# Performance work log

Hardware: AMD Instinct MI355X
Metric: run time of the kernel (lower is better)

## Reference

```python
import jax, jax.numpy as jnp
import numpy as np

S = 8192          # total tokens (8 images x 1024 patches)
DIM = 1280        # hidden_size
H = 16            # num_heads
DH = DIM // H     # head_dim = 80
N_SEG = 8         # number of image segments (equal-length)


def setup_inputs() -> dict:
    key = jax.random.key(0)
    ks = jax.random.split(key, 8)
    hidden_states = jax.random.normal(ks[0], (S, DIM), dtype=jnp.float32)
    ang = jax.random.uniform(ks[1], (S, DH), dtype=jnp.float32) * (2.0 * np.pi)
    cos = jnp.cos(ang)
    sin = jnp.sin(ang)
    cu_seqlens = (jnp.arange(N_SEG + 1, dtype=jnp.int32) * (S // N_SEG))
    qkv_w = jax.random.normal(ks[2], (3 * DIM, DIM), dtype=jnp.float32) * 0.02
    qkv_b = jax.random.normal(ks[3], (3 * DIM,), dtype=jnp.float32) * 0.02
    proj_w = jax.random.normal(ks[4], (DIM, DIM), dtype=jnp.float32) * 0.02
    proj_b = jax.random.normal(ks[5], (DIM,), dtype=jnp.float32) * 0.02
    return {
        "hidden_states": hidden_states,
        "cos": cos,
        "sin": sin,
        "qkv_w": qkv_w,
        "qkv_b": qkv_b,
        "proj_w": proj_w,
        "proj_b": proj_b,
        "cu_seqlens": cu_seqlens,
    }


def _rotate_half(x):
    d = x.shape[-1] // 2
    return jnp.concatenate([-x[..., d:], x[..., :d]], axis=-1)


def reference(hidden_states, cos, sin, qkv_w, qkv_b, proj_w, proj_b, cu_seqlens):
    s, dim = hidden_states.shape
    dh = cos.shape[-1]
    h = dim // dh
    n_seg = cu_seqlens.shape[0] - 1  # static; segments are equal-length
    L = s // n_seg
    scale = dh ** -0.5

    # fused QKV projection: [S, 3, H, DH]
    qkv = (hidden_states @ qkv_w.T + qkv_b).reshape(s, 3, h, dh)
    q, k, v = qkv[:, 0], qkv[:, 1], qkv[:, 2]

    # RoPE (fp32, broadcast cos/sin over heads)
    cos_b = cos[:, None, :].astype(jnp.float32)
    sin_b = sin[:, None, :].astype(jnp.float32)
    qf, kf = q.astype(jnp.float32), k.astype(jnp.float32)
    q = (qf * cos_b + _rotate_half(qf) * sin_b).astype(q.dtype)
    k = (kf * cos_b + _rotate_half(kf) * sin_b).astype(k.dtype)

    # per-segment (block-diagonal) attention: reshape to [n_seg, L, H, DH]
    qs = q.reshape(n_seg, L, h, dh)
    ks = k.reshape(n_seg, L, h, dh)
    vs = v.reshape(n_seg, L, h, dh)
    scores = jnp.einsum("glhd,gmhd->ghlm", qs, ks) * scale
    attn = jax.nn.softmax(scores, axis=-1)
    out = jnp.einsum("ghlm,gmhd->glhd", attn, vs).reshape(s, dim)
    return out @ proj_w.T + proj_b
```

## Files before the change

kernel.cpp:

```cpp
#include <hip/hip_runtime.h>
#include <hip/hip_bf16.h>
#include <stdint.h>

typedef unsigned short u16;
typedef unsigned int u32;
typedef __attribute__((ext_vector_type(8))) short short8;
typedef __attribute__((ext_vector_type(4))) float f32x4;

#define DEV __device__ __forceinline__

constexpr int S = 8192;
constexpr int DIM = 1280;
constexpr int H = 16;
constexpr int DH = 80;
constexpr int LSEG = 1024;
constexpr int QKVN = 3 * DIM;
constexpr float SCALE = 0.11180339887498949f * 1.4426950408889634f;

DEV u16 f2bf(float f) {
  u32 u = __float_as_uint(f);
  return (u16)((u + 0x7FFFu + ((u >> 16) & 1u)) >> 16);
}
DEV float bf2f(u16 h) { return __uint_as_float(((u32)h) << 16); }
DEV u32 pkbf(float a, float b) {
  __hip_bfloat162 t = __float22bfloat162_rn(float2{a, b});
  u32 r; __builtin_memcpy(&r, &t, 4); return r;
}

DEV void glds16(const void* g, void* l) {
  __builtin_amdgcn_global_load_lds((__attribute__((address_space(1))) void*)g,
                                   (__attribute__((address_space(3))) void*)l,
                                   16, 0, 0);
}
DEV f32x4 mfma16(short8 a, short8 b, f32x4 c) {
  return __builtin_amdgcn_mfma_f32_16x16x32_bf16(a, b, c, 0, 0, 0);
}

__global__ __launch_bounds__(256) void cvt_kernel(
    const float* __restrict__ X, const float* __restrict__ Wq,
    const float* __restrict__ Wp, u16* __restrict__ Xb,
    u16* __restrict__ Wqb, u16* __restrict__ Wpb) {
  size_t i = ((size_t)blockIdx.x * 256 + threadIdx.x) * 4;
  const size_t n1 = (size_t)S * DIM;
  const size_t n2 = (size_t)QKVN * DIM;
  const size_t n3 = (size_t)DIM * DIM;
  const float* src; u16* dst; size_t off;
  if (i < n1)                { src = X;  dst = Xb;  off = i; }
  else if (i < n1 + n2)      { src = Wq; dst = Wqb; off = i - n1; }
  else if (i < n1 + n2 + n3) { src = Wp; dst = Wpb; off = i - n1 - n2; }
  else return;
  float4 v = *(const float4*)(src + off);
  ushort4 r;
  r.x = f2bf(v.x); r.y = f2bf(v.y); r.z = f2bf(v.z); r.w = f2bf(v.w);
  *(ushort4*)(dst + off) = r;
}

__global__ __launch_bounds__(256) void rope_kernel(
    const u16* __restrict__ QKV, const float* __restrict__ cosp,
    const float* __restrict__ sinp, u16* __restrict__ Qp, u16* __restrict__ Kp) {
  int idx = blockIdx.x * 256 + threadIdx.x;
  int c = idx % 5;
  int sh = idx / 5;
  int s = sh >> 4, h = sh & 15;
  const size_t gbase = (size_t)s * QKVN + h * DH + c * 8;
  const size_t pbase = (size_t)sh * 96 + c * 8;
  short8 q0 = *(const short8*)&QKV[gbase];
  short8 q1 = *(const short8*)&QKV[gbase + 40];
  short8 k0 = *(const short8*)&QKV[gbase + DIM];
  short8 k1 = *(const short8*)&QKV[gbase + DIM + 40];
  float4 ca0 = *(const float4*)&cosp[s * DH + c * 8];
  float4 ca1 = *(const float4*)&cosp[s * DH + c * 8 + 4];
  float4 cb0 = *(const float4*)&cosp[s * DH + c * 8 + 40];
  float4 cb1 = *(const float4*)&cosp[s * DH + c * 8 + 44];
  float4 sa0 = *(const float4*)&sinp[s * DH + c * 8];
  float4 sa1 = *(const float4*)&sinp[s * DH + c * 8 + 4];
  float4 sb0 = *(const float4*)&sinp[s * DH + c * 8 + 40];
  float4 sb1 = *(const float4*)&sinp[s * DH + c * 8 + 44];
  float ca[8] = {ca0.x, ca0.y, ca0.z, ca0.w, ca1.x, ca1.y, ca1.z, ca1.w};
  float cb[8] = {cb0.x, cb0.y, cb0.z, cb0.w, cb1.x, cb1.y, cb1.z, cb1.w};
  float sa[8] = {sa0.x, sa0.y, sa0.z, sa0.w, sa1.x, sa1.y, sa1.z, sa1.w};
  float sb[8] = {sb0.x, sb0.y, sb0.z, sb0.w, sb1.x, sb1.y, sb1.z, sb1.w};
  short8 qo0, qo1, ko0, ko1;
#pragma unroll
  for (int j = 0; j < 8; j++) {
    float qa = bf2f((u16)q0[j]), qb = bf2f((u16)q1[j]);
    float ka = bf2f((u16)k0[j]), kb = bf2f((u16)k1[j]);
    qo0[j] = (short)f2bf((qa * ca[j] - qb * sa[j]) * SCALE);
    qo1[j] = (short)f2bf((qb * cb[j] + qa * sb[j]) * SCALE);
    ko0[j] = (short)f2bf(ka * ca[j] - kb * sa[j]);
    ko1[j] = (short)f2bf(kb * cb[j] + ka * sb[j]);
  }
  *(short8*)&Qp[pbase]      = qo0;
  *(short8*)&Qp[pbase + 40] = qo1;
  *(short8*)&Kp[pbase]      = ko0;
  *(short8*)&Kp[pbase + 40] = ko1;
  if (c == 0) {
    short8 z = {};
    *(short8*)&Qp[pbase + 80] = z; *(short8*)&Qp[pbase + 88] = z;
    *(short8*)&Kp[pbase + 80] = z; *(short8*)&Kp[pbase + 88] = z;
  }
}

__global__ __launch_bounds__(256) void vtrans_kernel(
    const u16* __restrict__ QKV, u16* __restrict__ Vt) {
  __shared__ u16 Ls[64 * 88];
  const int s0 = blockIdx.x * 64, h = blockIdx.y;
  const int tid = threadIdx.x;
  for (int cc = tid; cc < 640; cc += 256) {
    int row = cc / 10, c = cc % 10;
    short8 v = *(const short8*)&QKV[(size_t)(s0 + row) * QKVN + 2 * DIM + h * 80 + c * 8];
    *(short8*)&Ls[row * 88 + c * 8] = v;
  }
  __syncthreads();
  for (int cc = tid; cc < 640; cc += 256) {
    int d = cc / 8, sc = cc % 8;
    u16 tmp[8];
#pragma unroll
    for (int j = 0; j < 8; j++) {
      int op = sc * 8 + j;
      int key = ((op & 3) << 4) + (op >> 2);
      tmp[j] = Ls[key * 88 + d];
    }
    *(short8*)&Vt[(size_t)(h * 80 + d) * S + s0 + sc * 8] = *(short8*)tmp;
  }
}

template <bool OUT_F32>
__global__ __launch_bounds__(512, 2) void gemm_bt(
    const u16* __restrict__ A, const u16* __restrict__ B,
    const float* __restrict__ bias, void* __restrict__ C, int K, int N) {
  __shared__ u16 As[2][2][8192];
  __shared__ u16 Bs[2][2][8192];
  const int ntn = N >> 8;
  const int q = gridDim.x >> 3;
  const int widx = (blockIdx.x & 7) * q + (blockIdx.x >> 3);
  const int m0 = (widx / ntn) << 8;
  const int n0 = (widx % ntn) << 8;
  const int tid = threadIdx.x;
  const int w = tid >> 6, lane = tid & 63;
  const int quad = lane >> 4, l16 = lane & 15;
  const int wm = w >> 2, wn = w & 3;

  const int rowoff = w * 8 + (lane >> 3);
  const int coloff = ((lane & 7) ^ (lane >> 3)) * 8;
  const u16* pa0 = A + (size_t)(m0 + rowoff) * K + coloff;
  const u16* pa1 = A + (size_t)(m0 + 128 + rowoff) * K + coloff;
  const u16* pb0 = B + (size_t)(n0 + rowoff) * K + coloff;
  const u16* pb1 = B + (size_t)(n0 + 128 + rowoff) * K + coloff;
  const size_t j64 = (size_t)64 * K;

#define STG(P, DST, kk) do { \
    glds16((P) + (kk), &(DST)[w * 512]); \
    glds16((P) + j64 + (kk), &(DST)[4096 + w * 512]); } while (0)

  const int aro = (wm * 16 + l16) * 64;
  const int bro = (wn * 16 + l16) * 64;
  const int kc0 = ((quad) ^ (l16 & 7)) * 8;
  const int kc1 = ((4 + quad) ^ (l16 & 7)) * 8;

  float bv[4];
#pragma unroll
  for (int nf = 0; nf < 4; nf++) bv[nf] = bias[n0 + nf * 64 + wn * 16 + l16];

  f32x4 acc[8][4] = {};
  short8 af[4][2], bf0[2][2], bf1[2][2];
  const int NT = K >> 6;

  STG(pa0, As[0][0], 0);  STG(pb0, Bs[0][0], 0);
  STG(pa1, As[0][1], 0);  STG(pb1, Bs[0][1], 0);
  STG(pa0, As[1][0], 64); STG(pb0, Bs[1][0], 64);
  STG(pa1, As[1][1], 64); STG(pb1, Bs[1][1], 64);
  asm volatile("s_waitcnt vmcnt(8)" ::: "memory");
  asm volatile("s_barrier" ::: "memory");

  for (int t = 0; t < NT; ++t) {
    const int b = t & 1;
    const int kk2 = (t + 2) << 6;
    const bool pf = (t + 2 < NT);
#pragma unroll
    for (int i = 0; i < 4; i++) {
      af[i][0] = *(const short8*)&As[b][0][aro + i * 2048 + kc0];
      af[i][1] = *(const short8*)&As[b][0][aro + i * 2048 + kc1];
    }
#pragma unroll
    for (int jj = 0; jj < 2; jj++) {
      bf0[jj][0] = *(const short8*)&Bs[b][0][bro + jj * 4096 + kc0];
      bf0[jj][1] = *(const short8*)&Bs[b][0][bro + jj * 4096 + kc1];
    }
    asm volatile("s_barrier" ::: "memory");
    __builtin_amdgcn_s_setprio(1);
#pragma unroll
    for (int ks = 0; ks < 2; ks++)
#pragma unroll
      for (int i = 0; i < 4; i++)
#pragma unroll
        for (int jj = 0; jj < 2; jj++)
          acc[i][jj] = mfma16(af[i][ks], bf0[jj][ks], acc[i][jj]);
    __builtin_amdgcn_s_setprio(0);
    asm volatile("s_barrier" ::: "memory");
#pragma unroll
    for (int jj = 0; jj < 2; jj++) {
      bf1[jj][0] = *(const short8*)&Bs[b][1][bro + jj * 4096 + kc0];
      bf1[jj][1] = *(const short8*)&Bs[b][1][bro + jj * 4096 + kc1];
    }
    if (pf) { STG(pa0, As[b][0], kk2); STG(pb0, Bs[b][0], kk2); }
    asm volatile("s_barrier" ::: "memory");
    __builtin_amdgcn_s_setprio(1);
#pragma unroll
    for (int ks = 0; ks < 2; ks++)
#pragma unroll
      for (int i = 0; i < 4; i++)
#pragma unroll
        for (int jj = 0; jj < 2; jj++)
          acc[i][2 + jj] = mfma16(af[i][ks], bf1[jj][ks], acc[i][2 + jj]);
    __builtin_amdgcn_s_setprio(0);
    asm volatile("s_barrier" ::: "memory");
#pragma unroll
    for (int i = 0; i < 4; i++) {
      af[i][0] = *(const short8*)&As[b][1][aro + i * 2048 + kc0];
      af[i][1] = *(const short8*)&As[b][1][aro + i * 2048 + kc1];
    }
    if (pf) STG(pb1, Bs[b][1], kk2);
    asm volatile("s_barrier" ::: "memory");
    __builtin_amdgcn_s_setprio(1);
#pragma unroll
    for (int ks = 0; ks < 2; ks++)
#pragma unroll
      for (int i = 0; i < 4; i++)
#pragma unroll
        for (int jj = 0; jj < 2; jj++)
          acc[4 + i][jj] = mfma16(af[i][ks], bf0[jj][ks], acc[4 + i][jj]);
    __builtin_amdgcn_s_setprio(0);
    asm volatile("s_barrier" ::: "memory");
    if (pf) STG(pa1, As[b][1], kk2);
    __builtin_amdgcn_s_setprio(1);
#pragma unroll
    for (int ks = 0; ks < 2; ks++)
#pragma unroll
      for (int i = 0; i < 4; i++)
#pragma unroll
        for (int jj = 0; jj < 2; jj++)
          acc[4 + i][2 + jj] = mfma16(af[i][ks], bf1[jj][ks], acc[4 + i][2 + jj]);
    __builtin_amdgcn_s_setprio(0);
    if (t < NT - 2)       asm volatile("s_waitcnt vmcnt(8)" ::: "memory");
    else if (t == NT - 2) asm volatile("s_waitcnt vmcnt(0)" ::: "memory");
    asm volatile("s_barrier" ::: "memory");
  }
#undef STG
#pragma unroll
  for (int nf = 0; nf < 4; nf++) {
    int col = n0 + nf * 64 + wn * 16 + l16;
#pragma unroll
    for (int mf = 0; mf < 8; mf++) {
#pragma unroll
      for (int r = 0; r < 4; r++) {
        int row = m0 + mf * 32 + wm * 16 + quad * 4 + r;
        float v = acc[mf][nf][r] + bv[nf];
        if (OUT_F32) ((float*)C)[(size_t)row * N + col] = v;
        else         ((u16*)C)[(size_t)row * N + col] = f2bf(v);
      }
    }
  }
}

__global__ __launch_bounds__(256, 2) void attn_kernel(
    const u16* __restrict__ Qp, const u16* __restrict__ Kp,
    const u16* __restrict__ Vt, u16* __restrict__ O) {
  __shared__ u16 Ks[2][64 * 104];
  __shared__ u16 Vs[2][86 * 72];
  __shared__ u16 Ps[4][16 * 72];
  const int bid = blockIdx.x;
  const int phi = bid & 7, qt = (bid >> 3) & 7, pj = bid >> 6;
  const int p = pj * 8 + phi;
  const int g = p >> 4, h = p & 15;
  const int tid = threadIdx.x;
  const int w = tid >> 6, lane = tid & 63;
  const int quad = lane >> 4, l16 = lane & 15;

  short8 aq[2][3];
  const size_t qbase = ((size_t)(g * LSEG + qt * 128 + w * 32 + l16)) * 1536 + h * 96;
#pragma unroll
  for (int mt = 0; mt < 2; mt++)
#pragma unroll
    for (int ks = 0; ks < 3; ks++)
      aq[mt][ks] = *(const short8*)&Qp[qbase + (size_t)mt * 16 * 1536 + ks * 32 + quad * 8];

  const u16* gp[7]; u16* lp0[7]; u16* lp1[7]; int stp[7]; bool act[7];
#pragma unroll
  for (int i = 0; i < 7; i++) {
    int c = w + 4 * i;
    act[i] = (c < 25);
    int cc = act[i] ? c : 0;
    if (cc < 13) {
      int idx = cc * 64 + lane;
      int key = idx / 13, rc = idx % 13;
      int col = rc * 8; if (col >= 96) col = 0;
      gp[i] = Kp + (size_t)(g * LSEG + key) * 1536 + h * 96 + col;
      stp[i] = 64 * 1536;
      lp0[i] = &Ks[0][cc * 512]; lp1[i] = &Ks[1][cc * 512];
    } else {
      int cv = cc - 13;
      int idx = cv * 64 + lane;
      int d = idx / 9, rc = idx % 9;
      int col = rc * 8; if (col >= 64) col = 0;
      if (d >= 80) d = 0;
      gp[i] = Vt + (size_t)(h * 80 + d) * S + g * LSEG + col;
      stp[i] = 64;
      lp0[i] = &Vs[0][cv * 512]; lp1[i] = &Vs[1][cv * 512];
    }
  }
#pragma unroll
  for (int i = 0; i < 7; i++)
    if (act[i]) { glds16(gp[i], lp0[i]); gp[i] += stp[i]; }

  f32x4 o[2][5] = {};
  float lr[2][4] = {};
  u16* psw = &Ps[w][0];

  for (int kb = 0; kb < LSEG / 64; kb++) {
    const int b = kb & 1;
    __syncthreads();
    if (kb < LSEG / 64 - 1) {
      if (b == 0) {
#pragma unroll
        for (int i = 0; i < 7; i++)
          if (act[i]) { glds16(gp[i], lp1[i]); gp[i] += stp[i]; }
      } else {
#pragma unroll
        for (int i = 0; i < 7; i++)
          if (act[i]) { glds16(gp[i], lp0[i]); gp[i] += stp[i]; }
      }
    }
    f32x4 s[2][4] = {};
#pragma unroll
    for (int ks = 0; ks < 3; ks++) {
      short8 bk[4];
#pragma unroll
      for (int nt = 0; nt < 4; nt++)
        bk[nt] = *(const short8*)&Ks[b][(nt * 16 + l16) * 104 + ks * 32 + quad * 8];
#pragma unroll
      for (int mt = 0; mt < 2; mt++)
#pragma unroll
        for (int nt = 0; nt < 4; nt++)
          s[mt][nt] = mfma16(aq[mt][ks], bk[nt], s[mt][nt]);
    }
    short8 vb[5][2];
#pragma unroll
    for (int t = 0; t < 5; t++)
#pragma unroll
      for (int u = 0; u < 2; u++)
        vb[t][u] = *(const short8*)&Vs[b][(t * 16 + l16) * 72 + u * 32 + quad * 8];
#pragma unroll
    for (int mt = 0; mt < 2; mt++) {
#pragma unroll
      for (int r = 0; r < 4; r++) {
        float p0 = __builtin_amdgcn_exp2f(s[mt][0][r]);
        float p1 = __builtin_amdgcn_exp2f(s[mt][1][r]);
        float p2 = __builtin_amdgcn_exp2f(s[mt][2][r]);
        float p3 = __builtin_amdgcn_exp2f(s[mt][3][r]);
        lr[mt][r] += (p0 + p1) + (p2 + p3);
        int row = quad * 4 + r;
        uint2 pk; pk.x = pkbf(p0, p1); pk.y = pkbf(p2, p3);
        *(uint2*)&psw[row * 72 + l16 * 4] = pk;
      }
      short8 pa0 = *(const short8*)&psw[l16 * 72 + quad * 8];
      short8 pa1 = *(const short8*)&psw[l16 * 72 + 32 + quad * 8];
#pragma unroll
      for (int t = 0; t < 5; t++)
        o[mt][t] = mfma16(pa0, vb[t][0], o[mt][t]);
#pragma unroll
      for (int t = 0; t < 5; t++)
        o[mt][t] = mfma16(pa1, vb[t][1], o[mt][t]);
    }
  }
#pragma unroll
  for (int mt = 0; mt < 2; mt++)
#pragma unroll
    for (int r = 0; r < 4; r++) {
      float t = lr[mt][r];
#pragma unroll
      for (int off = 8; off >= 1; off >>= 1) t += __shfl_xor(t, off, 16);
      float inv = 1.f / t;
      int srow = g * LSEG + qt * 128 + w * 32 + mt * 16 + quad * 4 + r;
#pragma unroll
      for (int tt = 0; tt < 5; tt++)
        O[(size_t)srow * DIM + h * DH + tt * 16 + l16] = f2bf(o[mt][tt][r] * inv);
    }
}

extern "C" void kernel_launch(void* const* d_in, const int* in_sizes, int n_in,
                              void* d_out, int out_size, void* d_ws, size_t ws_size,
                              hipStream_t stream) {
  const float* X     = (const float*)d_in[0];
  const float* cosp  = (const float*)d_in[1];
  const float* sinp  = (const float*)d_in[2];
  const float* qkvw  = (const float*)d_in[3];
  const float* qkvb  = (const float*)d_in[4];
  const float* projw = (const float*)d_in[5];
  const float* projb = (const float*)d_in[6];
  float* out = (float*)d_out;

  u16* Xb   = (u16*)d_ws;
  u16* Wqb  = Xb   + (size_t)S * DIM;
  u16* Wpb  = Wqb  + (size_t)QKVN * DIM;
  u16* QKVb = Wpb  + (size_t)DIM * DIM;
  u16* Kp   = QKVb + (size_t)S * QKVN;
  u16* Vt   = Kp   + (size_t)S * H * 96;
  u16* Qp   = Xb;
  u16* AOb  = QKVb;

  cvt_kernel<<<16640, 256, 0, stream>>>(X, qkvw, projw, Xb, Wqb, Wpb);
  gemm_bt<false><<<(S / 256) * (QKVN / 256), 512, 0, stream>>>(Xb, Wqb, qkvb, QKVb, DIM, QKVN);
  rope_kernel<<<(S * H * 5) / 256, 256, 0, stream>>>(QKVb, cosp, sinp, Qp, Kp);
  vtrans_kernel<<<dim3(S / 64, H), 256, 0, stream>>>(QKVb, Vt);
  attn_kernel<<<1024, 256, 0, stream>>>(Qp, Kp, Vt, AOb);
  gemm_bt<true><<<(S / 256) * (DIM / 256), 512, 0, stream>>>(AOb, Wpb, projb, out, DIM, DIM);
}
```

Measured before the change: 335.8 us.

## Reschedule GEMM main loop to overlap LDS fragment loads with MFMA phases

Restructures the 256x256 GEMM inner loop so the B-fragment for the next tile is prefetched during the last MFMA phase. bf1 fragments are loaded together with A fragments before the first barrier, using explicit lgkmcnt waits instead of extra barriers. Global-to-LDS stages are issued right after barriers so they overlap the MFMA work. This removes one barrier per iteration and hides LDS latency, but the ordering of waits and buffer reuse is delicate and could introduce races if mis-scheduled.

```diff
diff --git a/kernel.cpp b/kernel.cpp
--- a/kernel.cpp
+++ b/kernel.cpp
@@ -152,6 +152,9 @@
 #define STG(P, DST, kk) do { \
     glds16((P) + (kk), &(DST)[w * 512]); \
     glds16((P) + j64 + (kk), &(DST)[4096 + w * 512]); } while (0)
+#define FENCE() asm volatile("" ::: "memory")
+#define BAR()   asm volatile("s_barrier" ::: "memory")
+#define LGKM(n) asm volatile("s_waitcnt lgkmcnt(" #n ")" ::: "memory")
 
   const int aro = (wm * 16 + l16) * 64;
   const int bro = (wn * 16 + l16) * 64;
@@ -161,17 +164,24 @@
   float bv[4];
 #pragma unroll
   for (int nf = 0; nf < 4; nf++) bv[nf] = bias[n0 + nf * 64 + wn * 16 + l16];
+  FENCE();
 
   f32x4 acc[8][4] = {};
   short8 af[4][2], bf0[2][2], bf1[2][2];
   const int NT = K >> 6;
 
   STG(pa0, As[0][0], 0);  STG(pb0, Bs[0][0], 0);
-  STG(pa1, As[0][1], 0);  STG(pb1, Bs[0][1], 0);
+  STG(pb1, Bs[0][1], 0);  STG(pa1, As[0][1], 0);
   STG(pa0, As[1][0], 64); STG(pb0, Bs[1][0], 64);
-  STG(pa1, As[1][1], 64); STG(pb1, Bs[1][1], 64);
+  STG(pb1, Bs[1][1], 64); STG(pa1, As[1][1], 64);
   asm volatile("s_waitcnt vmcnt(8)" ::: "memory");
-  asm volatile("s_barrier" ::: "memory");
+  BAR();
+#pragma unroll
+  for (int jj = 0; jj < 2; jj++) {
+    bf0[jj][0] = *(const short8*)&Bs[0][0][bro + jj * 4096 + kc0];
+    bf0[jj][1] = *(const short8*)&Bs[0][0][bro + jj * 4096 + kc1];
+  }
+  FENCE();
 
   for (int t = 0; t < NT; ++t) {
     const int b = t & 1;
@@ -184,10 +194,12 @@
     }
 #pragma unroll
     for (int jj = 0; jj < 2; jj++) {
-      bf0[jj][0] = *(const short8*)&Bs[b][0][bro + jj * 4096 + kc0];
-      bf0[jj][1] = *(const short8*)&Bs[b][0][bro + jj * 4096 + kc1];
-    }
-    asm volatile("s_barrier" ::: "memory");
+      bf1[jj][0] = *(const short8*)&Bs[b][1][bro + jj * 4096 + kc0];
+      bf1[jj][1] = *(const short8*)&Bs[b][1][bro + jj * 4096 + kc1];
+    }
+    LGKM(4);
+    BAR();
+    if (pf) { STG(pa0, As[b][0], kk2); STG(pb0, Bs[b][0], kk2); }
     __builtin_amdgcn_s_setprio(1);
 #pragma unroll
     for (int ks = 0; ks < 2; ks++)
@@ -197,14 +209,9 @@
         for (int jj = 0; jj < 2; jj++)
           acc[i][jj] = mfma16(af[i][ks], bf0[jj][ks], acc[i][jj]);
     __builtin_amdgcn_s_setprio(0);
-    asm volatile("s_barrier" ::: "memory");
-#pragma unroll
-    for (int jj = 0; jj < 2; jj++) {
-      bf1[jj][0] = *(const short8*)&Bs[b][1][bro + jj * 4096 + kc0];
-      bf1[jj][1] = *(const short8*)&Bs[b][1][bro + jj * 4096 + kc1];
-    }
-    if (pf) { STG(pa0, As[b][0], kk2); STG(pb0, Bs[b][0], kk2); }
-    asm volatile("s_barrier" ::: "memory");
+    LGKM(0);
+    BAR();
+    if (pf) STG(pb1, Bs[b][1], kk2);
     __builtin_amdgcn_s_setprio(1);
 #pragma unroll
     for (int ks = 0; ks < 2; ks++)
@@ -214,14 +221,15 @@
         for (int jj = 0; jj < 2; jj++)
           acc[i][2 + jj] = mfma16(af[i][ks], bf1[jj][ks], acc[i][2 + jj]);
     __builtin_amdgcn_s_setprio(0);
-    asm volatile("s_barrier" ::: "memory");
 #pragma unroll
     for (int i = 0; i < 4; i++) {
       af[i][0] = *(const short8*)&As[b][1][aro + i * 2048 + kc0];
       af[i][1] = *(const short8*)&As[b][1][aro + i * 2048 + kc1];
     }
-    if (pf) STG(pb1, Bs[b][1], kk2);
-    asm volatile("s_barrier" ::: "memory");
+    FENCE();
+    LGKM(0);
+    BAR();
+    if (pf) STG(pa1, As[b][1], kk2);
     __builtin_amdgcn_s_setprio(1);
 #pragma unroll
     for (int ks = 0; ks < 2; ks++)
@@ -231,8 +239,17 @@
         for (int jj = 0; jj < 2; jj++)
           acc[4 + i][jj] = mfma16(af[i][ks], bf0[jj][ks], acc[4 + i][jj]);
     __builtin_amdgcn_s_setprio(0);
-    asm volatile("s_barrier" ::: "memory");
-    if (pf) STG(pa1, As[b][1], kk2);
+    if (t < NT - 2)       asm volatile("s_waitcnt vmcnt(8)" ::: "memory");
+    else if (t == NT - 2) asm volatile("s_waitcnt vmcnt(0)" ::: "memory");
+    BAR();
+    if (t + 1 < NT) {
+#pragma unroll
+      for (int jj = 0; jj < 2; jj++) {
+        bf0[jj][0] = *(const short8*)&Bs[b ^ 1][0][bro + jj * 4096 + kc0];
+        bf0[jj][1] = *(const short8*)&Bs[b ^ 1][0][bro + jj * 4096 + kc1];
+      }
+      FENCE();
+    }
     __builtin_amdgcn_s_setprio(1);
 #pragma unroll
     for (int ks = 0; ks < 2; ks++)
@@ -242,11 +259,11 @@
         for (int jj = 0; jj < 2; jj++)
           acc[4 + i][2 + jj] = mfma16(af[i][ks], bf1[jj][ks], acc[4 + i][2 + jj]);
     __builtin_amdgcn_s_setprio(0);
-    if (t < NT - 2)       asm volatile("s_waitcnt vmcnt(8)" ::: "memory");
-    else if (t == NT - 2) asm volatile("s_waitcnt vmcnt(0)" ::: "memory");
-    asm volatile("s_barrier" ::: "memory");
   }
 #undef STG
+#undef FENCE
+#undef BAR
+#undef LGKM
 #pragma unroll
   for (int nf = 0; nf < 4; nf++) {
     int col = n0 + nf * 64 + wn * 16 + l16;
```

Result: no change. 331.4 us (-1.3%).
